# Kernel tuning notes

Measured on AMD Instinct MI355X. Metric: run time of the kernel, lower is better.

The kernel has to match this reference:

```python
import jax, jax.numpy as jnp
import numpy as np

TOP_K = 2
ROUTED_SCALING = 1.0


def setup_inputs() -> dict:
    key = jax.random.key(0)
    k1, k2, k3, k4 = jax.random.split(key, 4)
    S, B, H = 1024, 2, 1024
    E, FFN = 8, 1408
    return {
        "hidden_states": jax.random.normal(k1, (S, B, H), dtype=jnp.float32),
        "gate_w": jax.random.normal(k2, (E, H), dtype=jnp.float32) * 0.02,
        "w1": jax.random.normal(k3, (E, H, 2 * FFN), dtype=jnp.float32) * 0.02,
        "w2": jax.random.normal(k4, (E, FFN, H), dtype=jnp.float32) * 0.02,
    }


def reference(hidden_states, gate_w, w1, w2):
    # hidden_states: [S, B, H] -> transpose(0,1) as in MoELayer.forward
    x = jnp.transpose(hidden_states, (1, 0, 2))  # [B, S, H]
    B, S, H = x.shape
    E = gate_w.shape[0]
    xt = x.reshape(-1, H)  # [T, H], T = B*S
    T = xt.shape[0]

    # --- TopKGate ('greedy', softmax scoring) ---
    scores = jax.nn.softmax(xt @ gate_w.T, axis=-1)  # [T, E]
    topk_w, topk_idx = jax.lax.top_k(scores, TOP_K)  # [T, K]
    # norm_topk_prob: normalize the top-k weights
    topk_w = topk_w / (jnp.sum(topk_w, axis=-1, keepdims=True) + 1e-20)
    topk_w = topk_w * ROUTED_SCALING

    # Sparse combine weights [T, E] (zero for non-selected experts)
    combine = jnp.zeros((T, E), dtype=xt.dtype)
    combine = combine.at[jnp.arange(T)[:, None], topk_idx].set(topk_w)

    # --- Experts: per-expert swiglu MLP, weighted combine ---
    # Equivalent math to dispatch -> per-expert grouped GEMM -> combine:
    # non-selected experts contribute with weight 0.
    out = jnp.zeros_like(xt)
    for e in range(E):
        h = xt @ w1[e]                      # [T, 2*FFN]
        g, u = jnp.split(h, 2, axis=-1)
        y = (jax.nn.silu(g) * u) @ w2[e]    # [T, H]
        out = out + combine[:, e:e + 1] * y

    out = out.reshape(B, S, H)
    return jnp.transpose(out, (1, 0, 2))  # back to [S, B, H]
```

## Files before the change

### kernel.cpp

```cpp
#include <hip/hip_runtime.h>
#include <hip/hip_bf16.h>

#define S_      1024
#define B_      2
#define H_      1024
#define E_      8
#define FFN_    1408
#define TWO_FFN 2816
#define T_      2048
#define MAXSLOTS 5120
#define NB_CONV 512
#define TSZ     (128 * 64)

typedef float  f32x4 __attribute__((ext_vector_type(4)));
typedef short  s16x8 __attribute__((ext_vector_type(8)));

__device__ __forceinline__ unsigned short f2bf(float f) {
    unsigned u = __float_as_uint(f);
    u += 0x7fffu + ((u >> 16) & 1u);
    return (unsigned short)(u >> 16);
}
__device__ __forceinline__ unsigned pk2(float a, float b) {
    __hip_bfloat162 h = __float22bfloat162_rn(make_float2(a, b));
    unsigned u; __builtin_memcpy(&u, &h, 4); return u;
}
__device__ __forceinline__ void async16(const void* g, void* l) {
    __builtin_amdgcn_global_load_lds(
        (const __attribute__((address_space(1))) unsigned int*)(unsigned long long)g,
        (__attribute__((address_space(3))) unsigned int*)(unsigned long long)l,
        16, 0, 0);
}
__device__ __forceinline__ size_t xrow_off(int t) {
    return (size_t)(t & (S_ - 1)) * (B_ * H_) + (size_t)(t >> 10) * H_;
}

__device__ __forceinline__ void load8(f32x4 v[8], const float* __restrict__ p, size_t C) {
#pragma unroll
    for (int j = 0; j < 8; j++) v[j] = *(const f32x4*)(p + (size_t)j * C);
}
__device__ __forceinline__ void stage_wr(const f32x4 v[8], unsigned* __restrict__ base,
                                         const int off[4]) {
#pragma unroll
    for (int i = 0; i < 4; i++) {
        uint4 q;
        q.x = pk2(v[0][i], v[1][i]);
        q.y = pk2(v[2][i], v[3][i]);
        q.z = pk2(v[4][i], v[5][i]);
        q.w = pk2(v[6][i], v[7][i]);
        *(uint4*)(base + off[i]) = q;
    }
}
__device__ __forceinline__ void mfma_step(const unsigned short* __restrict__ As,
                                          const unsigned short* __restrict__ Bs,
                                          f32x4 acc[4][4], int rowB, int colB, int lane) {
    int sw = (lane & 7) << 3;
#pragma unroll
    for (int kk = 0; kk < 64; kk += 32) {
        int kr = (kk + ((lane >> 4) << 3)) ^ sw;
        s16x8 af[4], bf[4];
#pragma unroll
        for (int mi = 0; mi < 4; mi++) af[mi] = *(const s16x8*)&As[(rowB + mi * 16 + (lane & 15)) * 64 + kr];
#pragma unroll
        for (int ni = 0; ni < 4; ni++) bf[ni] = *(const s16x8*)&Bs[(colB + ni * 16 + (lane & 15)) * 64 + kr];
#pragma unroll
        for (int mi = 0; mi < 4; mi++)
#pragma unroll
            for (int ni = 0; ni < 4; ni++)
                acc[mi][ni] = __builtin_amdgcn_mfma_f32_16x16x32_bf16(af[mi], bf[ni], acc[mi][ni], 0, 0, 0);
    }
}

__global__ void k_prep(const float* __restrict__ hs, const float* __restrict__ gw,
                       unsigned short* __restrict__ xb,
                       int* __restrict__ topkI, float* __restrict__ topkW) {
    int cb = blockIdx.x, tid = threadIdx.x;
    int wid = tid >> 6, lane = tid & 63;
    int t = cb * 4 + wid;
    const float* xr = hs + xrow_off(t);
    unsigned short* xo = xb + (size_t)t * H_;
    float acc[E_];
#pragma unroll
    for (int e = 0; e < E_; e++) acc[e] = 0.f;
#pragma unroll
    for (int p = 0; p < 4; p++) {
        int h = p * 256 + lane * 4;
        const float4 v = *(const float4*)(xr + h);
        unsigned short o[4] = { f2bf(v.x), f2bf(v.y), f2bf(v.z), f2bf(v.w) };
        *(uint2*)(xo + h) = *(const uint2*)o;
#pragma unroll
        for (int e = 0; e < E_; e++) {
            const float4 g = *(const float4*)(gw + e * H_ + h);
            acc[e] += v.x * g.x + v.y * g.y + v.z * g.z + v.w * g.w;
        }
    }
#pragma unroll
    for (int e = 0; e < E_; e++)
        for (int off = 32; off > 0; off >>= 1) acc[e] += __shfl_down(acc[e], off);
    if (lane == 0) {
        float l0 = -1e30f, l1 = -1e30f; int i0 = 0, i1 = 0;
#pragma unroll
        for (int e = 0; e < E_; e++) {
            float v = acc[e];
            if (v > l0)      { l1 = l0; i1 = i0; l0 = v; i0 = e; }
            else if (v > l1) { l1 = v;  i1 = e; }
        }
        float p1 = expf(l1 - l0);
        float w0 = 1.f / (1.f + p1);
        float w1s = 1.f - w0;
        topkI[2 * t] = i0; topkI[2 * t + 1] = i1;
        topkW[2 * t] = w0; topkW[2 * t + 1] = w1s;
    }
}

__global__ void k_routeassign(const int* __restrict__ topkI, const float* __restrict__ topkW,
                              int* __restrict__ ctrl, int* __restrict__ perm,
                              int* __restrict__ slotOfTok) {
    __shared__ int s_wcnt[4][E_];
    __shared__ int s_base[E_];
    __shared__ int s_cur[E_];
    int tid = threadIdx.x, wid = tid >> 6, lane = tid & 63;
    int cnt[E_];
#pragma unroll
    for (int j = 0; j < E_; j++) cnt[j] = 0;
    for (int i = tid; i < 2 * T_; i += 256) {
        int e = topkI[i];
#pragma unroll
        for (int j = 0; j < E_; j++) cnt[j] += (e == j);
    }
#pragma unroll
    for (int j = 0; j < E_; j++)
        for (int off = 32; off > 0; off >>= 1) cnt[j] += __shfl_down(cnt[j], off);
    if (lane == 0) {
#pragma unroll
        for (int j = 0; j < E_; j++) s_wcnt[wid][j] = cnt[j];
    }
    __syncthreads();
    if (tid == 0) {
        int b = 0;
        for (int e = 0; e < E_; e++) {
            int n = s_wcnt[0][e] + s_wcnt[1][e] + s_wcnt[2][e] + s_wcnt[3][e];
            int ntile = (n + 127) >> 7;
            s_base[e] = b;
            ctrl[40 + e] = ntile;
            ctrl[48 + e] = b;
            b += ntile * 128;
        }
#pragma unroll
        for (int e = 0; e < E_; e++) s_cur[e] = 0;
    }
    __syncthreads();
    for (int s = tid; s < MAXSLOTS; s += 256) perm[s] = 0;
    __syncthreads();
    for (int t = tid; t < T_; t += 256) {
#pragma unroll
        for (int k = 0; k < 2; k++) {
            int e = topkI[2 * t + k];
            int pos = atomicAdd(&s_cur[e], 1);
            int slot = s_base[e] + pos;
            perm[slot] = t;
            slotOfTok[2 * t + k] = slot;
        }
    }
}

__global__ __launch_bounds__(256) void k_gemm1(
    const unsigned short* __restrict__ xb, const float* __restrict__ w1,
    const int* __restrict__ ctrl, const int* __restrict__ perm,
    unsigned short* __restrict__ A2) {
    int b  = blockIdx.x;
    int p  = ((b >> 7) << 3) | (b & 7);
    int ti = (b >> 3) & 15;
    int e  = p / 22;
    int ct = p - e * 22;
    if (ti >= ctrl[40 + e]) return;
    int slot0 = ctrl[48 + e] + ti * 128;
    __shared__ __align__(16) unsigned short As[2 * TSZ];
    __shared__ __align__(16) unsigned short Bs[2 * TSZ];
    int tid = threadIdx.x, wid = tid >> 6, lane = tid & 63;

    const unsigned short* aPtr[4];
    int lAoff[4];
#pragma unroll
    for (int i = 0; i < 4; i++) {
        int c = (wid * 4 + i) * 64 + lane;
        int r = c >> 3;
        int qd = (c & 7) ^ (r & 7);
        int tok = perm[slot0 + r];
        aPtr[i] = xb + (size_t)tok * H_ + qd * 8;
        lAoff[i] = c * 8;
    }
    int h1 = tid >> 7, kp = (tid >> 4) & 7, nq = tid & 15;
    int rb = h1 * 64 + nq * 4;
    const float* bsrc = w1 + (size_t)e * (H_ * TWO_FFN)
                        + (h1 ? (FFN_ + ct * 64) : (ct * 64)) + nq * 4
                        + (size_t)(kp * 8) * TWO_FFN;
    int bwOff[4];
#pragma unroll
    for (int i = 0; i < 4; i++)
        bwOff[i] = (rb + i) * 32 + ((kp ^ ((rb + i) & 7)) << 2);

    f32x4 acc[4][4];
#pragma unroll
    for (int mi = 0; mi < 4; mi++)
#pragma unroll
        for (int ni = 0; ni < 4; ni++) acc[mi][ni] = (f32x4){0.f, 0.f, 0.f, 0.f};
    int wm = wid & 1, wn = wid >> 1;
    int rowB = wm * 64, colB = wn * 64;

    f32x4 bv[8];
    load8(bv, bsrc, TWO_FFN);
    stage_wr(bv, (unsigned*)Bs, bwOff);
#pragma unroll
    for (int i = 0; i < 4; i++) async16(aPtr[i], As + lAoff[i]);
    load8(bv, bsrc + (size_t)64 * TWO_FFN, TWO_FFN);
#pragma unroll
    for (int i = 0; i < 4; i++) async16(aPtr[i] + 64, As + TSZ + lAoff[i]);
    __syncthreads();

    int cur = 0;
#pragma unroll 1
    for (int s = 0; s < 16; s++) {
        mfma_step(As + cur * TSZ, Bs + cur * TSZ, acc, rowB, colB, lane);
        if (s == 15) break;
        stage_wr(bv, (unsigned*)(Bs + (cur ^ 1) * TSZ), bwOff);
        __syncthreads();
        if (s < 14) {
            size_t k2 = (size_t)(s + 2) * 64;
#pragma unroll
            for (int i = 0; i < 4; i++) async16(aPtr[i] + k2, As + cur * TSZ + lAoff[i]);
            load8(bv, bsrc + k2 * TWO_FFN, TWO_FFN);
        }
        cur ^= 1;
    }
    __syncthreads();
    float* upLds = (float*)As;
    if (wn == 1) {
#pragma unroll
        for (int mi = 0; mi < 4; mi++)
#pragma unroll
            for (int ni = 0; ni < 4; ni++)
#pragma unroll
                for (int r = 0; r < 4; r++) {
                    int m = rowB + mi * 16 + (lane >> 4) * 4 + r;
                    int u = ni * 16 + (lane & 15);
                    upLds[m * 64 + u] = acc[mi][ni][r];
                }
    }
    __syncthreads();
    if (wn == 0) {
#pragma unroll
        for (int mi = 0; mi < 4; mi++)
#pragma unroll
            for (int r = 0; r < 4; r++) {
                int m = rowB + mi * 16 + (lane >> 4) * 4 + r;
                unsigned short* arow = A2 + (size_t)(slot0 + m) * FFN_ + ct * 64;
#pragma unroll
                for (int ni = 0; ni < 4; ni++) {
                    int gl = ni * 16 + (lane & 15);
                    float g = acc[mi][ni][r];
                    float u = upLds[m * 64 + gl];
                    float s = g / (1.f + expf(-g));
                    arow[gl] = f2bf(s * u);
                }
            }
    }
}

__global__ __launch_bounds__(256) void k_gemm2(
    const unsigned short* __restrict__ A2, const float* __restrict__ w2,
    const int* __restrict__ ctrl, unsigned short* __restrict__ Yp) {
    int b  = blockIdx.x;
    int p  = ((b >> 7) << 3) | (b & 7);
    int ti = (b >> 3) & 15;
    int e  = p >> 4;
    int ct = (p >> 1) & 7;
    int ks = p & 1;
    if (ti >= ctrl[40 + e]) return;
    int slot0 = ctrl[48 + e] + ti * 128;
    __shared__ __align__(16) unsigned short As[2 * TSZ];
    __shared__ __align__(16) unsigned short Bs[2 * TSZ];
    int tid = threadIdx.x, wid = tid >> 6, lane = tid & 63;

    const unsigned short* aPtr[4];
    int lAoff[4];
#pragma unroll
    for (int i = 0; i < 4; i++) {
        int c = (wid * 4 + i) * 64 + lane;
        int r = c >> 3;
        int qd = (c & 7) ^ (r & 7);
        aPtr[i] = A2 + (size_t)(slot0 + r) * FFN_ + qd * 8;
        lAoff[i] = c * 8;
    }
    int h1 = tid >> 7, kp = (tid >> 4) & 7, nq = tid & 15;
    int rb = h1 * 64 + nq * 4;
    int kbeg = ks * (FFN_ / 2);
    const float* bsrc = w2 + (size_t)e * (FFN_ * H_)
                        + ct * 128 + h1 * 64 + nq * 4
                        + (size_t)(kp * 8 + kbeg) * H_;
    int bwOff[4];
#pragma unroll
    for (int i = 0; i < 4; i++)
        bwOff[i] = (rb + i) * 32 + ((kp ^ ((rb + i) & 7)) << 2);

    f32x4 acc[4][4];
#pragma unroll
    for (int mi = 0; mi < 4; mi++)
#pragma unroll
        for (int ni = 0; ni < 4; ni++) acc[mi][ni] = (f32x4){0.f, 0.f, 0.f, 0.f};
    int wm = wid & 1, wn = wid >> 1;
    int rowB = wm * 64, colB = wn * 64;

    f32x4 bv[8];
    load8(bv, bsrc, H_);
    stage_wr(bv, (unsigned*)Bs, bwOff);
#pragma unroll
    for (int i = 0; i < 4; i++) async16(aPtr[i] + kbeg, As + lAoff[i]);
    load8(bv, bsrc + (size_t)64 * H_, H_);
#pragma unroll
    for (int i = 0; i < 4; i++) async16(aPtr[i] + kbeg + 64, As + TSZ + lAoff[i]);
    __syncthreads();

    int cur = 0;
#pragma unroll 1
    for (int s = 0; s < 11; s++) {
        mfma_step(As + cur * TSZ, Bs + cur * TSZ, acc, rowB, colB, lane);
        if (s == 10) break;
        stage_wr(bv, (unsigned*)(Bs + (cur ^ 1) * TSZ), bwOff);
        __syncthreads();
        if (s < 9) {
            size_t k2 = (size_t)(s + 2) * 64;
#pragma unroll
            for (int i = 0; i < 4; i++) async16(aPtr[i] + kbeg + k2, As + cur * TSZ + lAoff[i]);
            load8(bv, bsrc + k2 * H_, H_);
        }
        cur ^= 1;
    }
    unsigned short* yp = Yp + (size_t)ks * MAXSLOTS * H_;
#pragma unroll
    for (int mi = 0; mi < 4; mi++)
#pragma unroll
        for (int r = 0; r < 4; r++) {
            int m = rowB + mi * 16 + (lane >> 4) * 4 + r;
#pragma unroll
            for (int ni = 0; ni < 4; ni++) {
                int n = colB + ni * 16 + (lane & 15);
                yp[(size_t)(slot0 + m) * H_ + ct * 128 + n] = f2bf(acc[mi][ni][r]);
            }
        }
}

__global__ void k_combine(const unsigned short* __restrict__ Yp, const int* __restrict__ slotOfTok,
                          const float* __restrict__ topkW, float* __restrict__ out) {
    int t = blockIdx.x;
    int h = threadIdx.x * 4;
    int sA = slotOfTok[2 * t], sB = slotOfTok[2 * t + 1];
    float wA = topkW[2 * t],   wB = topkW[2 * t + 1];
    const unsigned short* pA0 = Yp + (size_t)sA * H_ + h;
    const unsigned short* pA1 = Yp + ((size_t)MAXSLOTS + sA) * H_ + h;
    const unsigned short* pB0 = Yp + (size_t)sB * H_ + h;
    const unsigned short* pB1 = Yp + ((size_t)MAXSLOTS + sB) * H_ + h;
    unsigned short a0[4], a1[4], b0[4], b1[4];
    *(uint2*)a0 = *(const uint2*)pA0;
    *(uint2*)a1 = *(const uint2*)pA1;
    *(uint2*)b0 = *(const uint2*)pB0;
    *(uint2*)b1 = *(const uint2*)pB1;
    float4 r;
    float* rp = (float*)&r;
#pragma unroll
    for (int i = 0; i < 4; i++) {
        float av = __uint_as_float(((unsigned)a0[i]) << 16) + __uint_as_float(((unsigned)a1[i]) << 16);
        float bv = __uint_as_float(((unsigned)b0[i]) << 16) + __uint_as_float(((unsigned)b1[i]) << 16);
        rp[i] = wA * av + wB * bv;
    }
    *(float4*)(out + xrow_off(t) + h) = r;
}

extern "C" void kernel_launch(void* const* d_in, const int* in_sizes, int n_in,
                              void* d_out, int out_size, void* d_ws, size_t ws_size,
                              hipStream_t stream) {
    (void)in_sizes; (void)n_in; (void)ws_size; (void)out_size;
    const float* hs = (const float*)d_in[0];
    const float* gw = (const float*)d_in[1];
    const float* w1 = (const float*)d_in[2];
    const float* w2 = (const float*)d_in[3];
    float* out = (float*)d_out;
    char* ws = (char*)d_ws;

    int*            ctrl   = (int*)ws;
    int*            topkI  = (int*)(ws + (16u << 10));
    float*          topkW  = (float*)(ws + (48u << 10));
    int*            perm   = (int*)(ws + (80u << 10));
    int*            slotOfTok = (int*)(ws + (144u << 10));
    unsigned short* xb    = (unsigned short*)(ws + (1ull  << 20));
    unsigned short* A2    = (unsigned short*)(ws + (8ull  << 20));
    unsigned short* Yp    = (unsigned short*)(ws + (24ull << 20));

    k_prep<<<NB_CONV, 256, 0, stream>>>(hs, gw, xb, topkI, topkW);
    k_routeassign<<<1, 256, 0, stream>>>(topkI, topkW, ctrl, perm, slotOfTok);
    k_gemm1<<<dim3(22 * 128), 256, 0, stream>>>(xb, w1, ctrl, perm, A2);
    k_gemm2<<<dim3(16 * 128), 256, 0, stream>>>(A2, w2, ctrl, Yp);
    k_combine<<<2048, 256, 0, stream>>>(Yp, slotOfTok, topkW, out);
}
```

Baseline: 273.9 us.

## Single-buffer LDS tiles in expert GEMMs and raise occupancy via launch bounds

After: 314.4 us. 1.15x slower.

```diff
diff --git a/kernel.cpp b/kernel.cpp
--- a/kernel.cpp
+++ b/kernel.cpp
@@ -163,7 +163,7 @@
     }
 }
 
-__global__ __launch_bounds__(256) void k_gemm1(
+__global__ __launch_bounds__(256, 4) void k_gemm1(
     const unsigned short* __restrict__ xb, const float* __restrict__ w1,
     const int* __restrict__ ctrl, const int* __restrict__ perm,
     unsigned short* __restrict__ A2) {
@@ -174,8 +174,9 @@
     int ct = p - e * 22;
     if (ti >= ctrl[40 + e]) return;
     int slot0 = ctrl[48 + e] + ti * 128;
-    __shared__ __align__(16) unsigned short As[2 * TSZ];
-    __shared__ __align__(16) unsigned short Bs[2 * TSZ];
+    __shared__ __align__(16) unsigned short smem[2 * TSZ];
+    unsigned short* As = smem;
+    unsigned short* Bs = smem + TSZ;
     int tid = threadIdx.x, wid = tid >> 6, lane = tid & 63;
 
     const unsigned short* aPtr[4];
@@ -213,27 +214,22 @@
 #pragma unroll
     for (int i = 0; i < 4; i++) async16(aPtr[i], As + lAoff[i]);
     load8(bv, bsrc + (size_t)64 * TWO_FFN, TWO_FFN);
-#pragma unroll
-    for (int i = 0; i < 4; i++) async16(aPtr[i] + 64, As + TSZ + lAoff[i]);
-    __syncthreads();
-
-    int cur = 0;
+    __syncthreads();
+
 #pragma unroll 1
     for (int s = 0; s < 16; s++) {
-        mfma_step(As + cur * TSZ, Bs + cur * TSZ, acc, rowB, colB, lane);
+        mfma_step(As, Bs, acc, rowB, colB, lane);
         if (s == 15) break;
-        stage_wr(bv, (unsigned*)(Bs + (cur ^ 1) * TSZ), bwOff);
         __syncthreads();
-        if (s < 14) {
-            size_t k2 = (size_t)(s + 2) * 64;
-#pragma unroll
-            for (int i = 0; i < 4; i++) async16(aPtr[i] + k2, As + cur * TSZ + lAoff[i]);
-            load8(bv, bsrc + k2 * TWO_FFN, TWO_FFN);
-        }
-        cur ^= 1;
-    }
-    __syncthreads();
-    float* upLds = (float*)As;
+        stage_wr(bv, (unsigned*)Bs, bwOff);
+        size_t ka = (size_t)(s + 1) * 64;
+#pragma unroll
+        for (int i = 0; i < 4; i++) async16(aPtr[i] + ka, As + lAoff[i]);
+        if (s < 14) load8(bv, bsrc + (size_t)(s + 2) * 64 * TWO_FFN, TWO_FFN);
+        __syncthreads();
+    }
+    __syncthreads();
+    float* upLds = (float*)smem;
     if (wn == 1) {
 #pragma unroll
         for (int mi = 0; mi < 4; mi++)
@@ -266,7 +262,7 @@
     }
 }
 
-__global__ __launch_bounds__(256) void k_gemm2(
+__global__ __launch_bounds__(256, 4) void k_gemm2(
     const unsigned short* __restrict__ A2, const float* __restrict__ w2,
     const int* __restrict__ ctrl, unsigned short* __restrict__ Yp) {
     int b  = blockIdx.x;
@@ -277,8 +273,8 @@
     int ks = p & 1;
     if (ti >= ctrl[40 + e]) return;
     int slot0 = ctrl[48 + e] + ti * 128;
-    __shared__ __align__(16) unsigned short As[2 * TSZ];
-    __shared__ __align__(16) unsigned short Bs[2 * TSZ];
+    __shared__ __align__(16) unsigned short As[TSZ];
+    __shared__ __align__(16) unsigned short Bs[TSZ];
     int tid = threadIdx.x, wid = tid >> 6, lane = tid & 63;
 
     const unsigned short* aPtr[4];
@@ -316,24 +312,19 @@
 #pragma unroll
     for (int i = 0; i < 4; i++) async16(aPtr[i] + kbeg, As + lAoff[i]);
     load8(bv, bsrc + (size_t)64 * H_, H_);
-#pragma unroll
-    for (int i = 0; i < 4; i++) async16(aPtr[i] + kbeg + 64, As + TSZ + lAoff[i]);
-    __syncthreads();
-
-    int cur = 0;
+    __syncthreads();
+
 #pragma unroll 1
     for (int s = 0; s < 11; s++) {
-        mfma_step(As + cur * TSZ, Bs + cur * TSZ, acc, rowB, colB, lane);
+        mfma_step(As, Bs, acc, rowB, colB, lane);
         if (s == 10) break;
-        stage_wr(bv, (unsigned*)(Bs + (cur ^ 1) * TSZ), bwOff);
         __syncthreads();
-        if (s < 9) {
-            size_t k2 = (size_t)(s + 2) * 64;
-#pragma unroll
-            for (int i = 0; i < 4; i++) async16(aPtr[i] + kbeg + k2, As + cur * TSZ + lAoff[i]);
-            load8(bv, bsrc + k2 * H_, H_);
-        }
-        cur ^= 1;
+        stage_wr(bv, (unsigned*)Bs, bwOff);
+        size_t ka = (size_t)(s + 1) * 64;
+#pragma unroll
+        for (int i = 0; i < 4; i++) async16(aPtr[i] + kbeg + ka, As + lAoff[i]);
+        if (s < 9) load8(bv, bsrc + (size_t)(s + 2) * 64 * H_, H_);
+        __syncthreads();
     }
     unsigned short* yp = Yp + (size_t)ks * MAXSLOTS * H_;
 #pragma unroll
```
